# Performance work log

Measured on AMD Instinct MI355X. Metric: run time of the kernel, lower is better.

Reference implementation:

```python
import jax, jax.numpy as jnp
import numpy as np

SLOPE = 0.01  # LeakyReLU default negative_slope


def _lrelu(x):
    return jnp.where(x >= 0, x, SLOPE * x)


def _similarity(x, w0, w1, w2, w3, w4):
    # stack of bias-free 1x1 convs == channel contractions
    def c(h, w):
        return jnp.einsum('bchw,oc->bohw', h, w)
    h = _lrelu(c(x, w0))
    h = _lrelu(c(h, w1))
    h = _lrelu(c(h, w2))
    h = _lrelu(c(h, w3))
    return c(h, w4)  # [B,1,H,W]


def setup_inputs() -> dict:
    key = jax.random.key(0)
    ks = jax.random.split(key, 7)
    B, C, S = 32, 256, 4

    def kaiming(k, out_c, in_c):
        # kaiming_normal_ mode='fan_out' on a 1x1 conv: std = sqrt(2/out_c)
        return jax.random.normal(k, (out_c, in_c), jnp.float32) * np.sqrt(2.0 / out_c).astype(np.float32)

    return {
        'template_feature': jax.random.normal(ks[0], (B, C, S, S), jnp.float32),
        'candidate_feature': jax.random.normal(ks[1], (B, C, 20, 20), jnp.float32),
        'w0': kaiming(ks[2], 256, 512),
        'w1': kaiming(ks[3], 128, 256),
        'w2': kaiming(ks[4], 64, 128),
        'w3': kaiming(ks[5], 32, 64),
        'w4': kaiming(ks[6], 1, 32),
    }


def reference(template_feature, candidate_feature, w0, w1, w2, w3, w4):
    B, C, S, _ = template_feature.shape  # S == 4
    K = 17  # number of 4x4 patch positions per axis on a 20x20 map

    # ---- template branch ----
    # sum/(H*W) expanded == mean broadcast
    tmean = jnp.mean(template_feature, axis=(2, 3), keepdims=True)
    rep = jnp.concatenate(
        [jnp.broadcast_to(tmean, template_feature.shape), template_feature], axis=1)
    w = _similarity(rep, w0, w1, w2, w3, w4)               # [B,1,S,S]
    wn = jax.nn.softmax(w.reshape(B, -1), axis=1).reshape(B, 1, S, S)
    common_template = jnp.sum(template_feature * wn, axis=(2, 3), keepdims=True)  # [B,C,1,1]
    common_template = jnp.concatenate(
        [common_template, wn.reshape(B, -1, 1, 1)], axis=1)  # [B,C+16,1,1]

    # ---- candidate branch ----
    # torch Unfold(4,4) then view(B,C,4,4,17,17): cfa[b,c,i,j,y,x] = cand[b,c,y+i,x+j]
    patches = jnp.stack(
        [candidate_feature[:, :, i:i + K, j:j + K] for i in range(S) for j in range(S)],
        axis=2)                                             # [B,C,16,K,K]
    cfa = patches.reshape(B, C, S, S, K, K)
    cmean = jnp.mean(cfa, axis=(2, 3), keepdims=True)       # [B,C,1,1,K,K]
    rep_c = jnp.concatenate(
        [jnp.broadcast_to(cmean, cfa.shape), cfa], axis=1)  # [B,2C,S,S,K,K]
    rep_c = rep_c.transpose(0, 4, 5, 1, 2, 3).reshape(B * K * K, 2 * C, S, S)
    wc = _similarity(rep_c, w0, w1, w2, w3, w4)             # [B*K*K,1,S,S]
    wcn = jax.nn.softmax(wc.reshape(B * K * K, -1), axis=1)
    wcn = wcn.reshape(B, K, K, 1, S, S).transpose(0, 3, 4, 5, 1, 2)  # [B,1,S,S,K,K]
    common_candidate = jnp.sum(cfa * wcn, axis=(2, 3), keepdims=True)  # [B,C,1,1,K,K]

    return common_template, common_candidate
```

## Files before the change

### kernel.cpp

```cpp
#include <hip/hip_runtime.h>
#include <hip/hip_bf16.h>
#include <hip/hip_fp16.h>

typedef __attribute__((ext_vector_type(8))) _Float16 half8v;
typedef __attribute__((ext_vector_type(4))) float f32x4;

__device__ __align__(16) float g_w0T[256 * 512];
__device__ __align__(16) unsigned short g_wa0[32 * 8 * 64 * 8];
__device__ __align__(16) unsigned short g_wp1[8 * 8 * 64 * 8];
__device__ __align__(16) unsigned short g_wp2[4 * 4 * 64 * 8];
__device__ __align__(16) unsigned short g_wp3[2 * 2 * 64 * 8];

__device__ __forceinline__ float lrelu(float x) { return x >= 0.f ? x : 0.01f * x; }
__device__ __forceinline__ unsigned short f2hu(float x) {
    _Float16 h = (_Float16)x; return *(unsigned short*)&h;
}
__device__ __forceinline__ unsigned short f2us(float x) {
    __hip_bfloat16 h = __float2bfloat16(x); return *(unsigned short*)&h;
}
__device__ __forceinline__ float us2f(unsigned short u) {
    union { unsigned i; float f; } c; c.i = ((unsigned)u) << 16; return c.f;
}
__device__ __forceinline__ uint2 pack_h4(const f32x4& a) {
    unsigned short h[4];
#pragma unroll
    for (int i = 0; i < 4; ++i) h[i] = f2hu(lrelu(a[i]));
    uint2 r;
    r.x = (unsigned)h[0] | ((unsigned)h[1] << 16);
    r.y = (unsigned)h[2] | ((unsigned)h[3] << 16);
    return r;
}

__global__ __launch_bounds__(256) void prep_kernel(
    const float* __restrict__ w0, const float* __restrict__ w1,
    const float* __restrict__ w2, const float* __restrict__ w3)
{
    int id = blockIdx.x * 256 + threadIdx.x;
    int stride = gridDim.x * 256;
    for (int i = id; i < 256 * 512; i += stride) {
        int c = i >> 9, j = i & 511;
        g_w0T[i] = (j < 256) ? w0[j * 512 + c] : w0[(j - 256) * 512 + 256 + c];
    }
    for (int i = id; i < 32 * 8 * 64 * 8; i += stride) {
        int e = i & 7, l = (i >> 3) & 63, k0 = (i >> 9) & 7, jt = i >> 12;
        int c = k0 * 32 + ((l >> 4) * 8) + e;
        int j = jt * 16 + (l & 15);
        float v = (j < 256) ? w0[j * 512 + c] : w0[(j - 256) * 512 + 256 + c];
        g_wa0[i] = f2hu(v);
    }
    for (int i = id; i < 8 * 8 * 64 * 8; i += stride) {
        int e = i & 7, l = (i >> 3) & 63, k0 = (i >> 9) & 7, m = i >> 12;
        int oc = m * 16 + (l & 15), c = k0 * 32 + ((l >> 4) * 8) + e;
        g_wp1[i] = f2hu(w1[oc * 256 + c]);
    }
    for (int i = id; i < 4 * 4 * 64 * 8; i += stride) {
        int e = i & 7, l = (i >> 3) & 63, k0 = (i >> 9) & 3, m = i >> 11;
        int oc = m * 16 + (l & 15), c = k0 * 32 + ((l >> 4) * 8) + e;
        g_wp2[i] = f2hu(w2[oc * 128 + c]);
    }
    for (int i = id; i < 2 * 2 * 64 * 8; i += stride) {
        int e = i & 7, l = (i >> 3) & 63, k0 = (i >> 9) & 1, m = i >> 10;
        int oc = m * 16 + (l & 15), c = k0 * 32 + ((l >> 4) * 8) + e;
        g_wp3[i] = f2hu(w3[oc * 64 + c]);
    }
}

__global__ __launch_bounds__(256) void front_kernel(
    const float* __restrict__ cand, const float* __restrict__ tf,
    float* __restrict__ A0f, float* __restrict__ A0t,
    float* __restrict__ ctF, unsigned short* __restrict__ ctH, int mode)
{
    __shared__ __align__(16) char fsm[20736];
    int bid = blockIdx.x;
    int t = threadIdx.x;

    if (bid < 1664) {
        int xcd = bid & 7, s = bid >> 3;
        int l = t & 63, w = t >> 6;
        int col = l & 15, q = l >> 4;

        int b, jh, pixg, estride;
        const float* srcb;
        float* dstb;
        if (s < 200) {
            b = xcd * 4 + s / 50;
            int rest = s % 50;
            jh = rest / 25;
            int pq = rest % 25;
            pixg = pq * 16 + col;
            estride = 400;
            srcb = cand + (size_t)(b * 256 + q * 8) * 400 + pixg;
            dstb = A0f + ((size_t)(b * 400) + pixg) * 512 + jh * 256 + w * 64 + q * 4;
        } else {
            int s2 = s - 200;
            b = xcd * 4 + (s2 >> 1);
            jh = s2 & 1;
            pixg = col;
            estride = 16;
            srcb = tf + (size_t)(b * 256 + q * 8) * 16 + pixg;
            dstb = A0t + ((size_t)(b * 16) + pixg) * 512 + jh * 256 + w * 64 + q * 4;
        }

        const half8v* Ah = (const half8v*)g_wa0;
        f32x4 acc[4];
#pragma unroll
        for (int mt = 0; mt < 4; ++mt) acc[mt] = (f32x4){0.f, 0.f, 0.f, 0.f};

        float cur[8];
#pragma unroll
        for (int e = 0; e < 8; ++e) cur[e] = srcb[(size_t)e * estride];

#pragma unroll
        for (int k0 = 0; k0 < 8; ++k0) {
            float nxt[8];
            if (k0 < 7) {
                const float* cpn = srcb + (size_t)(k0 + 1) * 32 * estride;
#pragma unroll
                for (int e = 0; e < 8; ++e) nxt[e] = cpn[(size_t)e * estride];
            }
            half8v bv;
#pragma unroll
            for (int e = 0; e < 8; ++e) bv[e] = (_Float16)cur[e];
#pragma unroll
            for (int mt = 0; mt < 4; ++mt) {
                int jt = jh * 16 + w * 4 + mt;
                half8v ah = Ah[(jt * 8 + k0) * 64 + l];
                acc[mt] = __builtin_amdgcn_mfma_f32_16x16x32_f16(ah, bv, acc[mt], 0, 0, 0);
            }
            if (k0 < 7) {
#pragma unroll
                for (int e = 0; e < 8; ++e) cur[e] = nxt[e];
            }
        }
#pragma unroll
        for (int mt = 0; mt < 4; ++mt) {
            float4 st = { acc[mt][0], acc[mt][1], acc[mt][2], acc[mt][3] };
            *(float4*)(dstb + mt * 16) = st;
        }
    } else {
        if (mode == 0) return;
        float (*tile)[81] = (float(*)[81])fsm;
        int blk = bid - 1664;
        int b = blk / 20, rest = blk % 20;
        int cg = rest / 5, pg = rest % 5;
        const float* src = cand + ((size_t)(b * 256 + cg * 64)) * 400 + pg * 80;
#pragma unroll
        for (int k = 0; k < 20; ++k) {
            int idx = k * 256 + t;
            int c = idx / 80, pix = idx % 80;
            tile[c][pix] = src[(size_t)c * 400 + pix];
        }
        __syncthreads();
#pragma unroll
        for (int k = 0; k < 20; ++k) {
            int idx = k * 256 + t;
            int pix = idx >> 6, c = idx & 63;
            float v = tile[c][pix];
            size_t off = ((size_t)(b * 400 + pg * 80 + pix)) * 256 + cg * 64 + c;
            if (mode == 2) ctF[off] = v;
            else           ctH[off] = f2us(v);
        }
    }
}

__global__ __launch_bounds__(256) void m0_kernel(
    const float* __restrict__ A0f, float* __restrict__ M0)
{
    int bid = blockIdx.x;
    int b = bid / 17, y = bid % 17;
    int t = threadIdx.x;
    const float* base = A0f + (size_t)b * 400 * 512;
    float cs[20];
#pragma unroll
    for (int xx = 0; xx < 20; ++xx) {
        float s = 0.f;
#pragma unroll
        for (int dy = 0; dy < 4; ++dy)
            s += base[(size_t)((y + dy) * 20 + xx) * 512 + t];
        cs[xx] = s;
    }
#pragma unroll
    for (int x = 0; x < 17; ++x) {
        float v = (cs[x] + cs[x + 1] + cs[x + 2] + cs[x + 3]) * 0.0625f;
        M0[((size_t)(b * 289 + y * 17 + x)) * 256 + t] = v;
    }
}

__global__ __launch_bounds__(512) void persist_kernel(
    const float* __restrict__ cand, const float* __restrict__ tf,
    const float* __restrict__ w4,
    const float* __restrict__ A0, const float* __restrict__ A0t,
    float* __restrict__ out,
    const float* __restrict__ ctF, const unsigned short* __restrict__ ctH, int mode,
    const float* __restrict__ M0, int use_m0k)
{
    __shared__ __align__(16) char smem[118784];
    const int WA1 = 0, WA2 = 65536, WA3 = 81920, STG = 86016;
    int t = threadIdx.x, l = t & 63, w = t >> 6;

    {
        uint4* d1 = (uint4*)(smem + WA1); const uint4* s1 = (const uint4*)g_wp1;
        for (int i = t; i < 4096; i += 512) d1[i] = s1[i];
        uint4* d2 = (uint4*)(smem + WA2); const uint4* s2 = (const uint4*)g_wp2;
        for (int i = t; i < 1024; i += 512) d2[i] = s2[i];
        uint4* d3 = (uint4*)(smem + WA3); const uint4* s3 = (const uint4*)g_wp3;
        for (int i = t; i < 256; i += 512) d3[i] = s3[i];
    }
    __syncthreads();

    char* bufA = smem + STG + w * 4096;
    char* bufB = bufA + 2048;
    const half8v* A1 = (const half8v*)(smem + WA1);
    const half8v* A2 = (const half8v*)(smem + WA2);
    const half8v* A3 = (const half8v*)(smem + WA3);

    int bid = blockIdx.x;
    int xcd = bid & 7, slot = bid >> 3;
    int p_ = l & 15, q = l >> 4;

    for (int j = slot * 8 + w; j < 1160; j += 256) {
        bool is_t = (j >= 1156);
        int b, r = 0;
        const float* afb;
        int pixo[16];
        if (!is_t) {
            int idx = xcd * 1156 + j;
            b = idx / 289; r = idx % 289;
            int y = r / 17, x = r % 17;
            afb = A0 + (size_t)b * 400 * 512;
#pragma unroll
            for (int p = 0; p < 16; ++p) pixo[p] = (y + (p >> 2)) * 20 + x + (p & 3);
        } else {
            b = xcd * 4 + (j - 1156);
            afb = A0t + (size_t)b * 16 * 512;
#pragma unroll
            for (int p = 0; p < 16; ++p) pixo[p] = p;
        }

        float m0q[4];
        bool m0_reg = (!is_t && use_m0k);
        if (m0_reg) {
            const float* mp = M0 + (size_t)(b * 289 + r) * 256 + l;
#pragma unroll
            for (int qt = 0; qt < 4; ++qt) m0q[qt] = mp[qt * 64];
        } else {
            float4 ms = {0.f, 0.f, 0.f, 0.f};
#pragma unroll
            for (int p = 0; p < 16; ++p) {
                float4 v = *(const float4*)(afb + (size_t)pixo[p] * 512 + 4 * l);
                ms.x += v.x; ms.y += v.y; ms.z += v.z; ms.w += v.w;
            }
            ms.x *= 0.0625f; ms.y *= 0.0625f; ms.z *= 0.0625f; ms.w *= 0.0625f;
            *(float4*)(bufB + l * 16) = ms;
        }

        float pxl[16];
#pragma unroll
        for (int p = 0; p < 16; ++p) pxl[p] = afb[(size_t)pixo[p] * 512 + 256 + l];

        f32x4 acc[8];
#pragma unroll
        for (int m = 0; m < 8; ++m) acc[m] = (f32x4){0.f, 0.f, 0.f, 0.f};

#pragma unroll
        for (int qt = 0; qt < 4; ++qt) {
            float m0c = m0_reg ? m0q[qt] : *(const float*)(bufB + (qt * 64 + l) * 4);
#pragma unroll
            for (int p = 0; p < 16; ++p) {
                float h = lrelu(m0c + pxl[p]);
                int off = p * 128 + ((((l >> 3) ^ (p & 7))) << 4) + (l & 7) * 2;
                *(unsigned short*)(bufA + off) = f2hu(h);
            }
            if (qt < 3) {
#pragma unroll
                for (int p = 0; p < 16; ++p)
                    pxl[p] = afb[(size_t)pixo[p] * 512 + 256 + (qt + 1) * 64 + l];
            }
#pragma unroll
            for (int kk = 0; kk < 2; ++kk) {
                int off = p_ * 128 + ((((kk * 4 + q) ^ (p_ & 7))) << 4);
                half8v bq = *(const half8v*)(bufA + off);
                int k0g = qt * 2 + kk;
#pragma unroll
                for (int m = 0; m < 8; ++m) {
                    half8v ah = A1[(m * 8 + k0g) * 64 + l];
                    acc[m] = __builtin_amdgcn_mfma_f32_16x16x32_f16(ah, bq, acc[m], 0, 0, 0);
                }
            }
        }

        f32x4 acc2[4];
#pragma unroll
        for (int m2 = 0; m2 < 4; ++m2) acc2[m2] = (f32x4){0.f, 0.f, 0.f, 0.f};

#pragma unroll
        for (int half = 0; half < 2; ++half) {
#pragma unroll
            for (int mm = 0; mm < 4; ++mm) {
                uint2 ph = pack_h4(acc[half * 4 + mm]);
                int off = p_ * 128 + ((((mm * 2 + (q >> 1)) ^ (p_ & 7))) << 4) + (q & 1) * 8;
                *(uint2*)(bufB + off) = ph;
            }
#pragma unroll
            for (int kf = 0; kf < 2; ++kf) {
                int off = p_ * 128 + ((((kf * 4 + q) ^ (p_ & 7))) << 4);
                half8v bq = *(const half8v*)(bufB + off);
                int kfg = half * 2 + kf;
#pragma unroll
                for (int m2 = 0; m2 < 4; ++m2) {
                    half8v ah = A2[(m2 * 4 + kfg) * 64 + l];
                    acc2[m2] = __builtin_amdgcn_mfma_f32_16x16x32_f16(ah, bq, acc2[m2], 0, 0, 0);
                }
            }
        }

#pragma unroll
        for (int m2 = 0; m2 < 4; ++m2) {
            uint2 ph = pack_h4(acc2[m2]);
            int off = p_ * 128 + ((((m2 * 2 + (q >> 1)) ^ (p_ & 7))) << 4) + (q & 1) * 8;
            *(uint2*)(bufA + off) = ph;
        }
        f32x4 acc3[2];
        acc3[0] = (f32x4){0.f, 0.f, 0.f, 0.f};
        acc3[1] = (f32x4){0.f, 0.f, 0.f, 0.f};
#pragma unroll
        for (int k0 = 0; k0 < 2; ++k0) {
            int off = p_ * 128 + ((((k0 * 4 + q) ^ (p_ & 7))) << 4);
            half8v bq = *(const half8v*)(bufA + off);
#pragma unroll
            for (int mt = 0; mt < 2; ++mt) {
                half8v ah = A3[(mt * 2 + k0) * 64 + l];
                acc3[mt] = __builtin_amdgcn_mfma_f32_16x16x32_f16(ah, bq, acc3[mt], 0, 0, 0);
            }
        }

        float s4 = 0.f;
#pragma unroll
        for (int mt = 0; mt < 2; ++mt)
#pragma unroll
            for (int rg = 0; rg < 4; ++rg)
                s4 += w4[mt * 16 + q * 4 + rg] * lrelu(acc3[mt][rg]);
        s4 += __shfl_xor(s4, 16); s4 += __shfl_xor(s4, 32);
        float mx = s4;
#pragma unroll
        for (int msk = 8; msk; msk >>= 1) mx = fmaxf(mx, __shfl_xor(mx, msk));
        float e = __expf(s4 - mx), sum = e;
#pragma unroll
        for (int msk = 8; msk; msk >>= 1) sum += __shfl_xor(sum, msk);
        float wnl = e / sum;
        if (l < 16) *(float*)(bufB + l * 4) = wnl;
        float wnv[16];
#pragma unroll
        for (int p = 0; p < 16; ++p) wnv[p] = *(const float*)(bufB + p * 4);

        if (is_t) {
            if (l < 16) out[b * 272 + 256 + l] = wnl;
#pragma unroll
            for (int ii = 0; ii < 4; ++ii) {
                int ch = ii * 64 + l;
                const float* tp = tf + (size_t)(b * 256 + ch) * 16;
                float a = 0.f;
#pragma unroll
                for (int p = 0; p < 16; ++p) a += tp[p] * wnv[p];
                out[b * 272 + ch] = a;
            }
        } else if (mode == 2) {
            const float* ct = ctF + (size_t)b * 400 * 256;
#pragma unroll
            for (int ii = 0; ii < 4; ++ii) {
                float a = 0.f;
#pragma unroll
                for (int p = 0; p < 16; ++p)
                    a += ct[(size_t)pixo[p] * 256 + ii * 64 + l] * wnv[p];
                out[8704 + (size_t)(b * 256 + ii * 64 + l) * 289 + r] = a;
            }
        } else if (mode == 1) {
            const unsigned short* ct = ctH + (size_t)b * 400 * 256;
#pragma unroll
            for (int ii = 0; ii < 4; ++ii) {
                float a = 0.f;
#pragma unroll
                for (int p = 0; p < 16; ++p)
                    a += us2f(ct[(size_t)pixo[p] * 256 + ii * 64 + l]) * wnv[p];
                out[8704 + (size_t)(b * 256 + ii * 64 + l) * 289 + r] = a;
            }
        } else {
            const float* cb = cand + (size_t)b * 256 * 400;
#pragma unroll
            for (int ii = 0; ii < 4; ++ii) {
                int ch = ii * 64 + l;
                const float* cp = cb + (size_t)ch * 400;
                float a = 0.f;
#pragma unroll
                for (int p = 0; p < 16; ++p) a += cp[pixo[p]] * wnv[p];
                out[8704 + (size_t)(b * 256 + ch) * 289 + r] = a;
            }
        }
    }
}

extern "C" void kernel_launch(void* const* d_in, const int* in_sizes, int n_in,
                              void* d_out, int out_size, void* d_ws, size_t ws_size,
                              hipStream_t stream)
{
    const float* tf = (const float*)d_in[0];
    const float* cf = (const float*)d_in[1];
    const float* w0 = (const float*)d_in[2];
    const float* w1 = (const float*)d_in[3];
    const float* w2 = (const float*)d_in[4];
    const float* w3 = (const float*)d_in[5];
    const float* w4 = (const float*)d_in[6];
    float* out = (float*)d_out;

    const size_t A0_BYTES  = (size_t)32 * 400 * 512 * 4;
    const size_t A0T_BYTES = (size_t)32 * 16 * 512 * 4;
    const size_t CT_F32    = (size_t)32 * 400 * 256 * 4;
    const size_t CT_BF16   = (size_t)32 * 400 * 256 * 2;
    const size_t M0_BYTES  = (size_t)32 * 289 * 256 * 4;

    float* A0f = (float*)d_ws;
    float* A0t = (float*)((char*)d_ws + A0_BYTES);
    char*  ctb = (char*)d_ws + A0_BYTES + A0T_BYTES;

    int mode = 0, use_m0k = 0;
    if (ws_size >= A0_BYTES + A0T_BYTES + CT_F32)       mode = 2;
    else if (ws_size >= A0_BYTES + A0T_BYTES + CT_BF16) mode = 1;
    if (mode == 2 && ws_size >= A0_BYTES + A0T_BYTES + CT_F32 + M0_BYTES) use_m0k = 1;
    float*          ctF = (float*)ctb;
    unsigned short* ctH = (unsigned short*)ctb;
    float*          M0  = (float*)(ctb + CT_F32);

    prep_kernel<<<680, 256, 0, stream>>>(w0, w1, w2, w3);
    front_kernel<<<2304, 256, 0, stream>>>(cf, tf, A0f, A0t, ctF, ctH, mode);
    if (use_m0k) m0_kernel<<<544, 256, 0, stream>>>(A0f, M0);
    persist_kernel<<<256, 512, 0, stream>>>(cf, tf, w4, A0f, A0t, out, ctF, ctH, mode, M0, use_m0k);
}
```

Measured before the change: 93.39 us.

## Shrink LDS footprint: load layer-2/3 weights from global, single per-wave buffer

Drops the shared-memory copies of the layer-2 and layer-3 packed weights and reads them straight from global memory (relying on cache), and merges the two per-wave staging buffers into one 2KB buffer. LDS use falls from about 116KB to 80KB. The mean computation now stays in registers instead of going through LDS, and the launch bound gains a min-blocks hint. The aim is more resident waves or fewer LDS transactions, at the cost of global/L2 latency on the A2/A3 loads inside the MFMA loops and possible register pressure from the bounds hint.

After: 230.7 us. 147% more time.

```diff
diff --git a/kernel.cpp b/kernel.cpp
--- a/kernel.cpp
+++ b/kernel.cpp
@@ -186,7 +186,7 @@
     }
 }
 
-__global__ __launch_bounds__(512) void persist_kernel(
+__global__ __launch_bounds__(512, 4) void persist_kernel(
     const float* __restrict__ cand, const float* __restrict__ tf,
     const float* __restrict__ w4,
     const float* __restrict__ A0, const float* __restrict__ A0t,
@@ -194,25 +194,20 @@
     const float* __restrict__ ctF, const unsigned short* __restrict__ ctH, int mode,
     const float* __restrict__ M0, int use_m0k)
 {
-    __shared__ __align__(16) char smem[118784];
-    const int WA1 = 0, WA2 = 65536, WA3 = 81920, STG = 86016;
+    __shared__ __align__(16) char smem[81920];
+    const int WA1 = 0, STG = 65536;
     int t = threadIdx.x, l = t & 63, w = t >> 6;
 
     {
         uint4* d1 = (uint4*)(smem + WA1); const uint4* s1 = (const uint4*)g_wp1;
         for (int i = t; i < 4096; i += 512) d1[i] = s1[i];
-        uint4* d2 = (uint4*)(smem + WA2); const uint4* s2 = (const uint4*)g_wp2;
-        for (int i = t; i < 1024; i += 512) d2[i] = s2[i];
-        uint4* d3 = (uint4*)(smem + WA3); const uint4* s3 = (const uint4*)g_wp3;
-        for (int i = t; i < 256; i += 512) d3[i] = s3[i];
     }
     __syncthreads();
 
-    char* bufA = smem + STG + w * 4096;
-    char* bufB = bufA + 2048;
+    char* buf = smem + STG + w * 2048;
     const half8v* A1 = (const half8v*)(smem + WA1);
-    const half8v* A2 = (const half8v*)(smem + WA2);
-    const half8v* A3 = (const half8v*)(smem + WA3);
+    const half8v* A2 = (const half8v*)g_wp2;
+    const half8v* A3 = (const half8v*)g_wp3;
 
     int bid = blockIdx.x;
     int xcd = bid & 7, slot = bid >> 3;
@@ -238,20 +233,19 @@
         }
 
         float m0q[4];
-        bool m0_reg = (!is_t && use_m0k);
-        if (m0_reg) {
+        if (!is_t && use_m0k) {
             const float* mp = M0 + (size_t)(b * 289 + r) * 256 + l;
 #pragma unroll
             for (int qt = 0; qt < 4; ++qt) m0q[qt] = mp[qt * 64];
         } else {
-            float4 ms = {0.f, 0.f, 0.f, 0.f};
-#pragma unroll
-            for (int p = 0; p < 16; ++p) {
-                float4 v = *(const float4*)(afb + (size_t)pixo[p] * 512 + 4 * l);
-                ms.x += v.x; ms.y += v.y; ms.z += v.z; ms.w += v.w;
-            }
-            ms.x *= 0.0625f; ms.y *= 0.0625f; ms.z *= 0.0625f; ms.w *= 0.0625f;
-            *(float4*)(bufB + l * 16) = ms;
+#pragma unroll
+            for (int qt = 0; qt < 4; ++qt) {
+                float s = 0.f;
+#pragma unroll
+                for (int p = 0; p < 16; ++p)
+                    s += afb[(size_t)pixo[p] * 512 + qt * 64 + l];
+                m0q[qt] = s * 0.0625f;
+            }
         }
 
         float pxl[16];
@@ -264,12 +258,12 @@
 
 #pragma unroll
         for (int qt = 0; qt < 4; ++qt) {
-            float m0c = m0_reg ? m0q[qt] : *(const float*)(bufB + (qt * 64 + l) * 4);
+            float m0c = m0q[qt];
 #pragma unroll
             for (int p = 0; p < 16; ++p) {
                 float h = lrelu(m0c + pxl[p]);
                 int off = p * 128 + ((((l >> 3) ^ (p & 7))) << 4) + (l & 7) * 2;
-                *(unsigned short*)(bufA + off) = f2hu(h);
+                *(unsigned short*)(buf + off) = f2hu(h);
             }
             if (qt < 3) {
 #pragma unroll
@@ -279,7 +273,7 @@
 #pragma unroll
             for (int kk = 0; kk < 2; ++kk) {
                 int off = p_ * 128 + ((((kk * 4 + q) ^ (p_ & 7))) << 4);
-                half8v bq = *(const half8v*)(bufA + off);
+                half8v bq = *(const half8v*)(buf + off);
                 int k0g = qt * 2 + kk;
 #pragma unroll
                 for (int m = 0; m < 8; ++m) {
@@ -299,12 +293,12 @@
             for (int mm = 0; mm < 4; ++mm) {
                 uint2 ph = pack_h4(acc[half * 4 + mm]);
                 int off = p_ * 128 + ((((mm * 2 + (q >> 1)) ^ (p_ & 7))) << 4) + (q & 1) * 8;
-                *(uint2*)(bufB + off) = ph;
+                *(uint2*)(buf + off) = ph;
             }
 #pragma unroll
             for (int kf = 0; kf < 2; ++kf) {
                 int off = p_ * 128 + ((((kf * 4 + q) ^ (p_ & 7))) << 4);
-                half8v bq = *(const half8v*)(bufB + off);
+                half8v bq = *(const half8v*)(buf + off);
                 int kfg = half * 2 + kf;
 #pragma unroll
                 for (int m2 = 0; m2 < 4; ++m2) {
@@ -318,7 +312,7 @@
         for (int m2 = 0; m2 < 4; ++m2) {
             uint2 ph = pack_h4(acc2[m2]);
             int off = p_ * 128 + ((((m2 * 2 + (q >> 1)) ^ (p_ & 7))) << 4) + (q & 1) * 8;
-            *(uint2*)(bufA + off) = ph;
+            *(uint2*)(buf + off) = ph;
         }
         f32x4 acc3[2];
         acc3[0] = (f32x4){0.f, 0.f, 0.f, 0.f};
@@ -326,7 +320,7 @@
 #pragma unroll
         for (int k0 = 0; k0 < 2; ++k0) {
             int off = p_ * 128 + ((((k0 * 4 + q) ^ (p_ & 7))) << 4);
-            half8v bq = *(const half8v*)(bufA + off);
+            half8v bq = *(const half8v*)(buf + off);
 #pragma unroll
             for (int mt = 0; mt < 2; ++mt) {
                 half8v ah = A3[(mt * 2 + k0) * 64 + l];
@@ -348,10 +342,10 @@
 #pragma unroll
         for (int msk = 8; msk; msk >>= 1) sum += __shfl_xor(sum, msk);
         float wnl = e / sum;
-        if (l < 16) *(float*)(bufB + l * 4) = wnl;
+        if (l < 16) *(float*)(buf + l * 4) = wnl;
         float wnv[16];
 #pragma unroll
-        for (int p = 0; p < 16; ++p) wnv[p] = *(const float*)(bufB + p * 4);
+        for (int p = 0; p < 16; ++p) wnv[p] = *(const float*)(buf + p * 4);
 
         if (is_t) {
             if (l < 16) out[b * 272 + 256 + l] = wnl;
```
